# Performance work log

Measured on AMD Instinct MI355X. Metric: run time of the kernel, lower is better.

Reference implementation:

```python
import jax, jax.numpy as jnp
import numpy as np

RC = 5.0
P = 6
N_ATOM = 4
N_AXIS = 8
EPS = 1e-5
C_RES = 0.89442719  # sqrt(0.8)
C_NEW = 0.4472      # ~sqrt(0.2)
BESSEL_PREF = float(np.sqrt(2.0 / RC))


def poly_cutoff(x):
    # nequip-style PolynomialCutoff, p=6
    xr = x / RC
    p = float(P)
    out = (1.0
           - (p + 1.0) * (p + 2.0) / 2.0 * xr ** P
           + p * (p + 2.0) * xr ** (P + 1)
           - p * (p + 1.0) / 2.0 * xr ** (P + 2))
    return jnp.where(xr < 1.0, out, 0.0)


def bessel(x, w):
    # x: [E], w: [n_basis] (trainable n*pi weights)
    return BESSEL_PREF * jnp.sin(w * x[:, None] / RC) / x[:, None]


def layer_norm(x, g, b):
    m = jnp.mean(x, axis=-1, keepdims=True)
    v = jnp.var(x, axis=-1, keepdims=True)
    return (x - m) * jax.lax.rsqrt(v + EPS) * g + b


def mlp3(x, W1, b1, W2, b2, W3, b3):
    # FFN: hidden block (linear-tanh-linear) + tanh + final linear
    h = jnp.tanh(x @ W1 + b1)
    h = jnp.tanh(h @ W2 + b2)
    return h @ W3 + b3


def resnet3(x, W1, b1, W2, b2, W3, b3):
    # ResNet: residual added where in/out dims match (final 64->64 linear)
    h = jnp.tanh(x @ W1 + b1)
    h = h @ W2 + b2
    return jnp.tanh(h) @ W3 + b3 + h


def seg_mean(x, idx, n):
    s = jax.ops.segment_sum(x, idx, num_segments=n)
    c = jax.ops.segment_sum(jnp.ones((x.shape[0],), x.dtype), idx, num_segments=n)
    c = jnp.maximum(c, 1.0).reshape((n,) + (1,) * (x.ndim - 1))
    return s / c


def setup_inputs() -> dict:
    key = jax.random.key(0)
    ks = iter(jax.random.split(key, 64))
    N, E, E2 = 40000, 320000, 160000
    NB, NR, NS, NA = 16, 64, 16, 8
    D = NA * NS  # 128 = n_hidden
    L = 2
    f32 = jnp.float32

    def nrm(shape, s=0.05):
        return jax.random.normal(next(ks), shape, dtype=f32) * s

    inp = {}
    inp['atom_types'] = jax.random.randint(next(ks), (N,), 0, N_ATOM, dtype=jnp.int32)
    ev = jax.random.normal(next(ks), (E, 3), dtype=f32)
    inp['env_vectors'] = ev
    inp['env_length'] = jnp.linalg.norm(ev, axis=-1) + 0.1
    inp['edge_length'] = jax.random.uniform(next(ks), (E2,), dtype=f32) * 4.0 + 0.5
    inp['env_index'] = jax.random.randint(next(ks), (2, E), 0, N, dtype=jnp.int32)
    inp['edge_index'] = jax.random.randint(next(ks), (2, E2), 0, N, dtype=jnp.int32)
    inp['bessel_w'] = jnp.arange(1, NB + 1, dtype=f32) * jnp.pi
    A = 2 * N_ATOM + NB  # 24
    inp['sr_W1'], inp['sr_b1'] = nrm((A, 64)), nrm((64,))
    inp['sr_W2'], inp['sr_b2'] = nrm((64, 64)), nrm((64,))
    inp['sr_W3'], inp['sr_b3'] = nrm((64, NS)), nrm((NS,))
    inp['rd_W1'], inp['rd_b1'] = nrm((A, 64)), nrm((64,))
    inp['rd_W2'], inp['rd_b2'] = nrm((64, 64)), nrm((64,))
    inp['rd_W3'], inp['rd_b3'] = nrm((64, NR)), nrm((NR,))
    inp['ne_emb_W'], inp['ne_emb_b'] = nrm((NR, D)), nrm((D,))
    inp['ne_nln_g'], inp['ne_nln_b'] = jnp.ones((D,), f32), jnp.zeros((D,), f32)
    inp['ne_eln_g'], inp['ne_eln_b'] = jnp.ones((NR,), f32), jnp.zeros((NR,), f32)
    inp['ly_emb_W'], inp['ly_emb_b'] = nrm((L, NR, D)), nrm((L, D))
    inp['ly_hid_W1'], inp['ly_hid_b1'] = nrm((L, 2 * D, 128)), nrm((L, 128))
    inp['ly_hid_W2'], inp['ly_hid_b2'] = nrm((L, 128, 128)), nrm((L, 128))
    inp['ly_hid_W3'], inp['ly_hid_b3'] = nrm((L, 128, D)), nrm((L, D))
    inp['ly_rdl_W1'], inp['ly_rdl_b1'] = nrm((L, NR + D, 64)), nrm((L, 64))
    inp['ly_rdl_W2'], inp['ly_rdl_b2'] = nrm((L, 64, 64)), nrm((L, 64))
    inp['ly_rdl_W3'], inp['ly_rdl_b3'] = nrm((L, 64, NR)), nrm((L, NR))
    inp['ly_nln_g'], inp['ly_nln_b'] = jnp.ones((L, D), f32), jnp.zeros((L, D), f32)
    inp['ly_eln_g'], inp['ly_eln_b'] = jnp.ones((L, NR), f32), jnp.zeros((L, NR), f32)
    return inp


def reference(atom_types, env_vectors, env_length, edge_length, env_index, edge_index,
              bessel_w,
              sr_W1, sr_b1, sr_W2, sr_b2, sr_W3, sr_b3,
              rd_W1, rd_b1, rd_W2, rd_b2, rd_W3, rd_b3,
              ne_emb_W, ne_emb_b, ne_nln_g, ne_nln_b, ne_eln_g, ne_eln_b,
              ly_emb_W, ly_emb_b,
              ly_hid_W1, ly_hid_b1, ly_hid_W2, ly_hid_b2, ly_hid_W3, ly_hid_b3,
              ly_rdl_W1, ly_rdl_b1, ly_rdl_W2, ly_rdl_b2, ly_rdl_W3, ly_rdl_b3,
              ly_nln_g, ly_nln_b, ly_eln_g, ly_eln_b):
    N = atom_types.shape[0]
    oh = jax.nn.one_hot(atom_types, N_ATOM, dtype=env_vectors.dtype)
    # atom_attr[index].transpose(1,0).reshape(E,-1) == concat of the two endpoints' one-hots
    env_attr = jnp.concatenate([oh[env_index[0]], oh[env_index[1]]], -1)   # [E, 2*n_atom]
    edge_attr = jnp.concatenate([oh[edge_index[0]], oh[edge_index[1]]], -1)
    ud_env = poly_cutoff(env_length)[:, None]    # [E, 1]
    ud_edge = poly_cutoff(edge_length)[:, None]  # [E2, 1]
    feat_env = jnp.concatenate([env_attr, ud_env * bessel(env_length, bessel_w)], -1)
    feat_edge = jnp.concatenate([edge_attr, ud_edge * bessel(edge_length, bessel_w)], -1)
    env_sqrt = mlp3(feat_env, sr_W1, sr_b1, sr_W2, sr_b2, sr_W3, sr_b3) * ud_env  # [E, n_sqrt]
    env_radial = layer_norm(mlp3(feat_env, rd_W1, rd_b1, rd_W2, rd_b2, rd_W3, rd_b3), ne_eln_g, ne_eln_b) * ud_env
    edge_radial = layer_norm(mlp3(feat_edge, rd_W1, rd_b1, rd_W2, rd_b2, rd_W3, rd_b3), ne_eln_g, ne_eln_b) * ud_edge
    # SE(2) aggregation: msg = [env_sqrt | ud * env_vectors]; outer product per node
    msg = env_sqrt[:, :, None] * (ud_env * env_vectors)[:, None, :]  # [E, n_sqrt, 3]
    agg = seg_mean(msg, env_index[1], N)                             # [N, n_sqrt, 3]
    gram = jnp.einsum('nds,nes->nde', agg, agg)[:, :, :N_AXIS]       # [N, n_sqrt, n_axis]
    node_emb = layer_norm(gram.reshape(N, -1), ne_nln_g, ne_nln_b)   # [N, D]
    env_hidden = (env_radial @ ne_emb_W + ne_emb_b) * (node_emb[env_index[1]] + node_emb[env_index[0]]) * 0.5
    edge_hidden = (edge_radial @ ne_emb_W + ne_emb_b) * (node_emb[edge_index[1]] + node_emb[edge_index[0]]) * 0.5
    for l in range(ly_emb_W.shape[0]):
        env_weight = env_radial @ ly_emb_W[l] + ly_emb_b[l]  # [E, D]
        agg2 = seg_mean(env_weight * node_emb[env_index[1]], env_index[1], N)
        node_emb = C_RES * node_emb + C_NEW * layer_norm(agg2, ly_nln_g[l], ly_nln_b[l])
        env_hidden = mlp3(jnp.concatenate([node_emb[env_index[0]], env_hidden], -1),
                          ly_hid_W1[l], ly_hid_b1[l], ly_hid_W2[l], ly_hid_b2[l], ly_hid_W3[l], ly_hid_b3[l])
        edge_hidden = mlp3(jnp.concatenate([node_emb[edge_index[0]], edge_hidden], -1),
                           ly_hid_W1[l], ly_hid_b1[l], ly_hid_W2[l], ly_hid_b2[l], ly_hid_W3[l], ly_hid_b3[l])
        env_radial = C_RES * env_radial + C_NEW * ud_env * layer_norm(
            resnet3(jnp.concatenate([env_radial, env_hidden], -1),
                    ly_rdl_W1[l], ly_rdl_b1[l], ly_rdl_W2[l], ly_rdl_b2[l], ly_rdl_W3[l], ly_rdl_b3[l]),
            ly_eln_g[l], ly_eln_b[l])
        edge_radial = C_RES * edge_radial + C_NEW * ud_edge * layer_norm(
            resnet3(jnp.concatenate([edge_radial, edge_hidden], -1),
                    ly_rdl_W1[l], ly_rdl_b1[l], ly_rdl_W2[l], ly_rdl_b2[l], ly_rdl_W3[l], ly_rdl_b3[l]),
            ly_eln_g[l], ly_eln_b[l])
    return env_radial, edge_radial, node_emb, env_hidden, edge_hidden
```

## Files before the change

### kernel.cpp

```cpp
#include <hip/hip_runtime.h>
#include <math.h>

#define C_RES 0.89442719f
#define C_NEW 0.4472f
#define LN_EPS 1e-5f
#define BESSEL_PREF 0.6324555320336759f
#define RC_INV 0.2f

typedef __attribute__((ext_vector_type(8))) short short8;
typedef __attribute__((ext_vector_type(8))) unsigned short u16x8;
typedef __attribute__((ext_vector_type(16))) float f32x16;

__device__ __forceinline__ float fast_tanh(float x) {
  float ax = fabsf(x);
  float e = __expf(2.0f * ax);
  float t = 1.0f - 2.0f / (e + 1.0f);
  return copysignf(t, x);
}

__device__ __forceinline__ unsigned short f2b(float f) {
  __bf16 h = (__bf16)f;
  return __builtin_bit_cast(unsigned short, h);
}

__device__ __forceinline__ float b2f(unsigned short v) {
  return __uint_as_float((unsigned)v << 16);
}

__device__ __forceinline__ u16x8 cvt8(const float* s) {
  const float4 v0 = *(const float4*)s;
  const float4 v1 = *(const float4*)(s + 4);
  u16x8 w;
  w[0]=f2b(v0.x); w[1]=f2b(v0.y); w[2]=f2b(v0.z); w[3]=f2b(v0.w);
  w[4]=f2b(v1.x); w[5]=f2b(v1.y); w[6]=f2b(v1.z); w[7]=f2b(v1.w);
  return w;
}

__device__ __forceinline__ short8 cvt8s(const float* s) {
  const float4 v0 = *(const float4*)s;
  const float4 v1 = *(const float4*)(s + 4);
  short8 w;
  w[0]=(short)f2b(v0.x); w[1]=(short)f2b(v0.y); w[2]=(short)f2b(v0.z); w[3]=(short)f2b(v0.w);
  w[4]=(short)f2b(v1.x); w[5]=(short)f2b(v1.y); w[6]=(short)f2b(v1.z); w[7]=(short)f2b(v1.w);
  return w;
}

__device__ __forceinline__ float poly_cutoff(float x) {
  float xr = x * RC_INV;
  if (xr >= 1.0f) return 0.0f;
  float x2 = xr * xr;
  float x3 = x2 * xr;
  float x6 = x3 * x3;
  return 1.0f - 28.0f * x6 + 48.0f * x6 * xr - 21.0f * x6 * x2;
}

__device__ __forceinline__ int swz(int s, int kc) {
  return s ^ ((s >> 5) << 1) ^ ((kc & 1) << 2);
}

__global__ void zero_int_kernel(int* __restrict__ p, int n) {
  int i = blockIdx.x * blockDim.x + threadIdx.x;
  int stride = gridDim.x * blockDim.x;
  for (; i < n; i += stride) p[i] = 0;
}


__global__ void hist_kernel(int E, const int* __restrict__ idx, int* __restrict__ ecnt) {
  int t = blockIdx.x * 256 + threadIdx.x;
  if (t < E) atomicAdd(&ecnt[idx[E + t]], 1);
}

__launch_bounds__(1024)
__global__ void scan_kernel(const int* __restrict__ ecnt, int* __restrict__ eoff,
                            int* __restrict__ ecur, int n) {
  __shared__ int wsum[16];
  __shared__ int carry;
  const int tid = threadIdx.x;
  const int lane = tid & 63, wid = tid >> 6;
  if (tid == 0) carry = 0;
  __syncthreads();
  for (int b0 = 0; b0 < n; b0 += 1024) {
    const int i = b0 + tid;
    const int v = (i < n) ? ecnt[i] : 0;
    int incl = v;
    #pragma unroll
    for (int o = 1; o < 64; o <<= 1) {
      const int t = __shfl_up(incl, o);
      if (lane >= o) incl += t;
    }
    if (lane == 63) wsum[wid] = incl;
    __syncthreads();
    if (wid == 0) {
      const int wv = (lane < 16) ? wsum[lane] : 0;
      int wsc = wv;
      #pragma unroll
      for (int o = 1; o < 16; o <<= 1) {
        const int t = __shfl_up(wsc, o);
        if (lane >= o) wsc += t;
      }
      if (lane < 16) wsum[lane] = wsc - wv;
    }
    __syncthreads();
    const int c0 = carry;
    const int excl = c0 + wsum[wid] + incl - v;
    if (i < n) { eoff[i] = excl; ecur[i] = excl; }
    __syncthreads();
    if (tid == 1023) carry = c0 + wsum[15] + incl;
    __syncthreads();
  }
  if (tid == 0) eoff[n] = carry;
}

__global__ void scatter_kernel(int E, const int* __restrict__ idx,
                               int* __restrict__ ecur, int* __restrict__ perm) {
  int t = blockIdx.x * 256 + threadIdx.x;
  if (t < E) {
    const int pos = atomicAdd(&ecur[idx[E + t]], 1);
    perm[pos] = t;
  }
}


__global__ void pack_hid_weights(const float* __restrict__ W1,
                                 const float* __restrict__ W2,
                                 const float* __restrict__ W3,
                                 unsigned short* __restrict__ out)
{
  int t = blockIdx.x * 256 + threadIdx.x;
  if (t >= 131072) return;
  int l = t >> 16;
  int oidx = t & 65535;
  const float* src;
  int midx;
  if (oidx < 32768)      { src = W1 + l * 32768; midx = oidx; }
  else if (oidx < 49152) { src = W2 + l * 16384; midx = oidx - 32768; }
  else                   { src = W3 + l * 16384; midx = oidx - 49152; }
  int j = midx & 7;
  int lane = (midx >> 3) & 63;
  int blk = midx >> 9;
  int ct = blk & 3, kc = blk >> 2;
  int col = ct * 32 + (lane & 31);
  int k = kc * 16 + (lane >> 5) * 8 + j;
  out[l * 65536 + oidx] = f2b(src[k * 128 + col]);
}

__global__ void pack_rdl_weights(const float* __restrict__ W1,
                                 const float* __restrict__ W2,
                                 const float* __restrict__ W3,
                                 unsigned short* __restrict__ out)
{
  int t = blockIdx.x * 256 + threadIdx.x;
  if (t >= 40960) return;
  int l = t / 20480;
  int o = t - l * 20480;
  const float* src;
  int midx;
  if (o < 12288)      { src = W1 + l * 12288; midx = o; }
  else if (o < 16384) { src = W2 + l * 4096;  midx = o - 12288; }
  else                { src = W3 + l * 4096;  midx = o - 16384; }
  int j = midx & 7;
  int lane = (midx >> 3) & 63;
  int blk = midx >> 9;
  int ct = blk & 1, kc = blk >> 1;
  int col = ct * 32 + (lane & 31);
  int k = kc * 16 + (lane >> 5) * 8 + j;
  out[l * 20480 + o] = f2b(src[k * 64 + col]);
}

__global__ void pack_feat_weights(const float* __restrict__ rdW1,
                                  const float* __restrict__ rdW2,
                                  const float* __restrict__ rdW3,
                                  const float* __restrict__ srW1,
                                  const float* __restrict__ srW2,
                                  const float* __restrict__ srW3,
                                  unsigned short* __restrict__ out)
{
  int t = blockIdx.x * 256 + threadIdx.x;
  if (t >= 18432) return;
  const int blk = t >> 9, midx = t & 511;
  const int j = midx & 7, lane = (midx >> 3) & 63;
  const float* src; int kc, ct, K, NC;
  if (blk < 4)       { int b = blk;      src = rdW1; kc = b>>1; ct = b&1; K = 24; NC = 64; }
  else if (blk < 12) { int b = blk - 4;  src = rdW2; kc = b>>1; ct = b&1; K = 64; NC = 64; }
  else if (blk < 20) { int b = blk - 12; src = rdW3; kc = b>>1; ct = b&1; K = 64; NC = 64; }
  else if (blk < 24) { int b = blk - 20; src = srW1; kc = b>>1; ct = b&1; K = 24; NC = 64; }
  else if (blk < 32) { int b = blk - 24; src = srW2; kc = b>>1; ct = b&1; K = 64; NC = 64; }
  else               { int b = blk - 32; src = srW3; kc = b;    ct = 0;   K = 64; NC = 16; }
  const int col = ct * 32 + (lane & 31);
  const int k = kc * 16 + (lane >> 5) * 8 + j;
  const float v = (k < K && col < NC) ? src[k * NC + col] : 0.0f;
  out[t] = f2b(v);
}

__global__ void pack_emb_weights(const float* __restrict__ W,
                                 unsigned short* __restrict__ out)
{
  int t = blockIdx.x * 256 + threadIdx.x;
  if (t >= 8192) return;
  const int j = t & 7, lane = (t >> 3) & 63, blk = t >> 9;
  const int ct = blk & 3, kc = blk >> 2;
  const int col = ct * 32 + (lane & 31);
  const int k = kc * 16 + (lane >> 5) * 8 + j;
  out[t] = f2b(W[k * 128 + col]);
}


#define FEAT_TRANS(BASEBLK, V0, V1) do {                                        \
    _Pragma("unroll")                                                           \
    for (int ct_ = 0; ct_ < 2; ++ct_) {                                         \
      const int colh_ = ct_*32 + cl;                                            \
      const int kc2_  = colh_ >> 4;                                             \
      const int b3_   = (colh_ >> 3) & 1;                                       \
      const int jj_   = colh_ & 7;                                              \
      const int blk_  = ((BASEBLK) + kc2_*3 + wave)*512;                        \
      _Pragma("unroll")                                                         \
      for (int q_ = 0; q_ < 16; ++q_) {                                         \
        const int row32_ = (q_ & 3) + 8*(q_ >> 2) + 4*(lane >> 5);              \
        const int s2_ = (row32_ & 31) + 32*b3_;                                 \
        const float v_ = ct_ ? (V1)[q_] : (V0)[q_];                             \
        afrag[blk_ + swz(s2_, kc2_)*8 + jj_] = f2b(fast_tanh(v_));              \
      }                                                                         \
    }                                                                           \
  } while (0)

__launch_bounds__(192)
__global__ void feat_mfma(
    int g1, int n1, const float* __restrict__ lens1, const int* __restrict__ idx1,
    float* __restrict__ radial1, float* __restrict__ ud1,
    int n2, const float* __restrict__ lens2, const int* __restrict__ idx2,
    float* __restrict__ radial2, float* __restrict__ ud2,
    const int* __restrict__ types, const float* __restrict__ vecs,
    const float* __restrict__ bessel_w,
    const unsigned short* __restrict__ wpackf,
    const float* __restrict__ srb1, const float* __restrict__ srb2,
    const float* __restrict__ srb3,
    const float* __restrict__ rdb1, const float* __restrict__ rdb2,
    const float* __restrict__ rdb3,
    const float* __restrict__ eln_g, const float* __restrict__ eln_b,
    float* __restrict__ msgbuf)
{
  __shared__ __align__(16) unsigned short afrag[30*512];
  __shared__ __align__(16) unsigned short wlds[36*512];
  __shared__ float udl[96];

  const int tid  = threadIdx.x;
  const int lane = tid & 63;
  const int wave = tid >> 6;
  const int cl   = lane & 31;

  int blk = blockIdx.x;
  const bool has_sr = (blk < g1);
  int nrows; const float* lens; const int* idx; float* radial_out; float* ud_out;
  if (has_sr) { nrows = n1; lens = lens1; idx = idx1; radial_out = radial1; ud_out = ud1; }
  else { blk -= g1; nrows = n2; lens = lens2; idx = idx2; radial_out = radial2; ud_out = ud2; }
  const int base = blk * 96;

  for (int i = tid; i < 2304; i += 192)
    *(u16x8*)&wlds[i*8] = *(const u16x8*)&wpackf[i*8];

  {
    const int r = tid >> 1, h = tid & 1;
    int rowc = base + r;
    const bool valid = rowc < nrows;
    if (!valid) rowc = nrows - 1;
    const int i0 = idx[rowc];
    const int i1 = idx[nrows + rowc];
    const float len = lens[rowc];
    const float ud = poly_cutoff(len);
    const int t0 = types[i0], t1 = types[i1];
    const float invl = 1.0f / len;
    const int rt = r >> 5;
    #pragma unroll
    for (int m = 0; m < 12; ++m) {
      const int k = h + m*2;
      float v;
      if (k < 4)      v = (t0 == k) ? 1.0f : 0.0f;
      else if (k < 8) v = (t1 == (k-4)) ? 1.0f : 0.0f;
      else            v = ud * BESSEL_PREF * __sinf(bessel_w[k-8] * len * RC_INV) * invl;
      const int kc = k >> 4;
      const int s_ = (r & 31) + 32*((k >> 3) & 1);
      afrag[(kc*3 + rt)*512 + swz(s_, kc)*8 + (k & 7)] = f2b(v);
    }
    #pragma unroll
    for (int m = 0; m < 4; ++m) {
      const int k = 24 + h + m*2;
      const int s_ = (r & 31) + 32*((k >> 3) & 1);
      afrag[(1*3 + rt)*512 + swz(s_, 1)*8 + (k & 7)] = 0;
    }
    if (h == 0) {
      udl[r] = ud;
      if (valid) {
        ud_out[rowc] = ud;
        if (has_sr) {
          msgbuf[(size_t)rowc*20 + 16] = ud * vecs[(size_t)rowc*3 + 0];
          msgbuf[(size_t)rowc*20 + 17] = ud * vecs[(size_t)rowc*3 + 1];
          msgbuf[(size_t)rowc*20 + 18] = ud * vecs[(size_t)rowc*3 + 2];
        }
      }
    }
  }
  __syncthreads();

  f32x16 acc0, acc1;

  {
    const float bv0 = rdb1[cl], bv1 = rdb1[32 + cl];
    #pragma unroll
    for (int q = 0; q < 16; ++q) { acc0[q] = bv0; acc1[q] = bv1; }
  }
  #pragma unroll
  for (int kc = 0; kc < 2; ++kc) {
    const short8 a  = *(const short8*)&afrag[(kc*3 + wave)*512 + swz(lane, kc)*8];
    const short8 w0 = *(const short8*)&wlds[(kc*2 + 0)*512 + lane*8];
    const short8 w1 = *(const short8*)&wlds[(kc*2 + 1)*512 + lane*8];
    acc0 = __builtin_amdgcn_mfma_f32_32x32x16_bf16(a, w0, acc0, 0, 0, 0);
    acc1 = __builtin_amdgcn_mfma_f32_32x32x16_bf16(a, w1, acc1, 0, 0, 0);
  }
  FEAT_TRANS(6, acc0, acc1);

  {
    const float bv0 = rdb2[cl], bv1 = rdb2[32 + cl];
    #pragma unroll
    for (int q = 0; q < 16; ++q) { acc0[q] = bv0; acc1[q] = bv1; }
  }
  #pragma unroll
  for (int kc = 0; kc < 4; ++kc) {
    const short8 a  = *(const short8*)&afrag[((6 + kc*3) + wave)*512 + swz(lane, kc)*8];
    const short8 w0 = *(const short8*)&wlds[(4 + kc*2 + 0)*512 + lane*8];
    const short8 w1 = *(const short8*)&wlds[(4 + kc*2 + 1)*512 + lane*8];
    acc0 = __builtin_amdgcn_mfma_f32_32x32x16_bf16(a, w0, acc0, 0, 0, 0);
    acc1 = __builtin_amdgcn_mfma_f32_32x32x16_bf16(a, w1, acc1, 0, 0, 0);
  }
  FEAT_TRANS(18, acc0, acc1);

  {
    const float bv0 = rdb3[cl], bv1 = rdb3[32 + cl];
    #pragma unroll
    for (int q = 0; q < 16; ++q) { acc0[q] = bv0; acc1[q] = bv1; }
  }
  #pragma unroll
  for (int kc = 0; kc < 4; ++kc) {
    const short8 a  = *(const short8*)&afrag[((18 + kc*3) + wave)*512 + swz(lane, kc)*8];
    const short8 w0 = *(const short8*)&wlds[(12 + kc*2 + 0)*512 + lane*8];
    const short8 w1 = *(const short8*)&wlds[(12 + kc*2 + 1)*512 + lane*8];
    acc0 = __builtin_amdgcn_mfma_f32_32x32x16_bf16(a, w0, acc0, 0, 0, 0);
    acc1 = __builtin_amdgcn_mfma_f32_32x32x16_bf16(a, w1, acc1, 0, 0, 0);
  }
  {
    const float eg0 = eln_g[cl],      eb0 = eln_b[cl];
    const float eg1 = eln_g[32 + cl], eb1 = eln_b[32 + cl];
    #pragma unroll
    for (int q = 0; q < 16; ++q) {
      const float v0 = acc0[q], v1 = acc1[q];
      float s = v0 + v1, ss = v0*v0 + v1*v1;
      #pragma unroll
      for (int o = 1; o <= 16; o <<= 1) {
        s  += __shfl_xor(s, o);
        ss += __shfl_xor(ss, o);
      }
      const float m   = s * (1.0f/64.0f);
      const float inv = rsqrtf(ss * (1.0f/64.0f) - m*m + LN_EPS);
      const int row32 = (q & 3) + 8*(q >> 2) + 4*(lane >> 5);
      const int rloc  = wave*32 + row32;
      const int row   = base + rloc;
      if (row < nrows) {
        const float u = udl[rloc];
        radial_out[(size_t)row*64 + cl]      = ((v0 - m)*inv*eg0 + eb0) * u;
        radial_out[(size_t)row*64 + 32 + cl] = ((v1 - m)*inv*eg1 + eb1) * u;
      }
    }
  }

  if (has_sr) {
    {
      const float bv0 = srb1[cl], bv1 = srb1[32 + cl];
      #pragma unroll
      for (int q = 0; q < 16; ++q) { acc0[q] = bv0; acc1[q] = bv1; }
    }
    #pragma unroll
    for (int kc = 0; kc < 2; ++kc) {
      const short8 a  = *(const short8*)&afrag[(kc*3 + wave)*512 + swz(lane, kc)*8];
      const short8 w0 = *(const short8*)&wlds[(20 + kc*2 + 0)*512 + lane*8];
      const short8 w1 = *(const short8*)&wlds[(20 + kc*2 + 1)*512 + lane*8];
      acc0 = __builtin_amdgcn_mfma_f32_32x32x16_bf16(a, w0, acc0, 0, 0, 0);
      acc1 = __builtin_amdgcn_mfma_f32_32x32x16_bf16(a, w1, acc1, 0, 0, 0);
    }
    FEAT_TRANS(6, acc0, acc1);

    {
      const float bv0 = srb2[cl], bv1 = srb2[32 + cl];
      #pragma unroll
      for (int q = 0; q < 16; ++q) { acc0[q] = bv0; acc1[q] = bv1; }
    }
    #pragma unroll
    for (int kc = 0; kc < 4; ++kc) {
      const short8 a  = *(const short8*)&afrag[((6 + kc*3) + wave)*512 + swz(lane, kc)*8];
      const short8 w0 = *(const short8*)&wlds[(24 + kc*2 + 0)*512 + lane*8];
      const short8 w1 = *(const short8*)&wlds[(24 + kc*2 + 1)*512 + lane*8];
      acc0 = __builtin_amdgcn_mfma_f32_32x32x16_bf16(a, w0, acc0, 0, 0, 0);
      acc1 = __builtin_amdgcn_mfma_f32_32x32x16_bf16(a, w1, acc1, 0, 0, 0);
    }
    FEAT_TRANS(18, acc0, acc1);

    {
      const float bv0 = (cl < 16) ? srb3[cl] : 0.0f;
      #pragma unroll
      for (int q = 0; q < 16; ++q) acc0[q] = bv0;
    }
    #pragma unroll
    for (int kc = 0; kc < 4; ++kc) {
      const short8 a  = *(const short8*)&afrag[((18 + kc*3) + wave)*512 + swz(lane, kc)*8];
      const short8 w0 = *(const short8*)&wlds[(32 + kc)*512 + lane*8];
      acc0 = __builtin_amdgcn_mfma_f32_32x32x16_bf16(a, w0, acc0, 0, 0, 0);
    }
    if (cl < 16) {
      #pragma unroll
      for (int q = 0; q < 16; ++q) {
        const int row32 = (q & 3) + 8*(q >> 2) + 4*(lane >> 5);
        const int rloc  = wave*32 + row32;
        const int row   = base + rloc;
        if (row < nrows) msgbuf[(size_t)row*20 + cl] = acc0[q] * udl[rloc];
      }
    }
  }
}


__launch_bounds__(256)
__global__ void msg_gather_kernel(int N, const int* __restrict__ eoff,
                                  const int* __restrict__ perm,
                                  const float* __restrict__ msgbuf,
                                  float* __restrict__ aggS)
{
  const int w = (blockIdx.x * 256 + threadIdx.x) >> 6;
  const int lane = threadIdx.x & 63;
  if (w >= N) return;
  const int s = eoff[w], e = eoff[w + 1];
  const int d = lane / 3, c = lane - d * 3;
  float acc = 0.0f;
  for (int j = s; j < e; ++j) {
    const int ed = perm[j];
    if (lane < 48)
      acc += msgbuf[(size_t)ed*20 + d] * msgbuf[(size_t)ed*20 + 16 + c];
  }
  if (lane < 48) aggS[(size_t)w*48 + lane] = acc;
}


__device__ __forceinline__ void block128_stats(float x, float& m, float& inv, float* red) {
  float s = x, ss = x*x;
  #pragma unroll
  for (int o = 32; o; o >>= 1) { s += __shfl_down(s, o); ss += __shfl_down(ss, o); }
  const int t = threadIdx.x;
  if ((t & 63) == 0) { red[(t >> 6)*2] = s; red[(t >> 6)*2 + 1] = ss; }
  __syncthreads();
  const float S = red[0] + red[2], SS = red[1] + red[3];
  m = S * (1.0f/128.0f);
  const float var = SS * (1.0f/128.0f) - m*m;
  inv = rsqrtf(var + LN_EPS);
}

__launch_bounds__(128)
__global__ void node_emb_kernel(int N, const float* __restrict__ aggS,
                                const int* __restrict__ ecnt,
                                const float* __restrict__ g, const float* __restrict__ b,
                                float* __restrict__ node_emb)
{
  const int n = blockIdx.x, t = threadIdx.x;
  __shared__ float S[48];
  __shared__ float red[4];
  if (t < 48) S[t] = aggS[(size_t)n*48 + t];
  __syncthreads();
  const float ic = 1.0f / fmaxf((float)ecnt[n], 1.0f);
  const int d = t >> 3, e = t & 7;
  const float x = (S[d*3+0]*S[e*3+0] + S[d*3+1]*S[e*3+1] + S[d*3+2]*S[e*3+2]) * ic * ic;
  float m, inv;
  block128_stats(x, m, inv, red);
  node_emb[(size_t)n*128 + t] = (x - m)*inv*g[t] + b[t];
}


__launch_bounds__(256)
__global__ void agg_gather_kernel(int N, const int* __restrict__ eoff,
                                  const int* __restrict__ perm,
                                  const float* __restrict__ radial,
                                  float* __restrict__ mean_r)
{
  const int w = (blockIdx.x * 256 + threadIdx.x) >> 6;
  const int lane = threadIdx.x & 63;
  if (w >= N) return;
  const int s = eoff[w], e = eoff[w + 1];
  float acc = 0.0f;
  for (int j = s; j < e; ++j) {
    const int ed = perm[j];
    acc += radial[(size_t)ed * 64 + lane];
  }
  const float inv = 1.0f / fmaxf((float)(e - s), 1.0f);
  mean_r[(size_t)w * 64 + lane] = acc * inv;
}


__launch_bounds__(256)
__global__ void node_update_gemm(
    int N, const float* __restrict__ mean_r, const int* __restrict__ ecnt,
    const float* __restrict__ W, const float* __restrict__ bias,
    const float* __restrict__ g, const float* __restrict__ b,
    float* __restrict__ node_emb)
{
  __shared__ __align__(16) float lw[64*128];
  __shared__ float lm[32][65];
  const int tid = threadIdx.x;
  const int base = blockIdx.x * 32;

  for (int i = tid; i < 8192; i += 256) lw[i] = W[i];
  {
    const int rr0 = tid >> 6, k = tid & 63;
    for (int rr = rr0; rr < 32; rr += 4) {
      const int n = base + rr;
      lm[rr][k] = (n < N) ? mean_r[(size_t)n*64 + k] : 0.0f;
    }
  }
  __syncthreads();

  const int r0 = (tid >> 5) * 4, j0 = (tid & 31) * 4;
  float acc[4][4];
  #pragma unroll
  for (int j = 0; j < 4; ++j) {
    const float bj = bias[j0 + j];
    acc[0][j] = bj; acc[1][j] = bj; acc[2][j] = bj; acc[3][j] = bj;
  }
  for (int k = 0; k < 64; ++k) {
    const float4 w = *(const float4*)&lw[k*128 + j0];
    const float s0 = lm[r0][k],   s1 = lm[r0+1][k];
    const float s2 = lm[r0+2][k], s3 = lm[r0+3][k];
    acc[0][0] += s0*w.x; acc[0][1] += s0*w.y; acc[0][2] += s0*w.z; acc[0][3] += s0*w.w;
    acc[1][0] += s1*w.x; acc[1][1] += s1*w.y; acc[1][2] += s1*w.z; acc[1][3] += s1*w.w;
    acc[2][0] += s2*w.x; acc[2][1] += s2*w.y; acc[2][2] += s2*w.z; acc[2][3] += s2*w.w;
    acc[3][0] += s3*w.x; acc[3][1] += s3*w.y; acc[3][2] += s3*w.z; acc[3][3] += s3*w.w;
  }

  const float g0 = g[j0], g1 = g[j0+1], g2 = g[j0+2], g3 = g[j0+3];
  const float bb0 = b[j0], bb1 = b[j0+1], bb2 = b[j0+2], bb3 = b[j0+3];
  #pragma unroll
  for (int i = 0; i < 4; ++i) {
    const int n = base + r0 + i;
    if (n >= N) continue;
    const float mask = (ecnt[n] > 0) ? 1.0f : 0.0f;
    const float4 old = *(const float4*)&node_emb[(size_t)n*128 + j0];
    const float x0 = old.x * acc[i][0] * mask;
    const float x1 = old.y * acc[i][1] * mask;
    const float x2 = old.z * acc[i][2] * mask;
    const float x3 = old.w * acc[i][3] * mask;
    float s = x0 + x1 + x2 + x3;
    float ss = x0*x0 + x1*x1 + x2*x2 + x3*x3;
    #pragma unroll
    for (int o = 1; o <= 16; o <<= 1) {
      s  += __shfl_xor(s, o);
      ss += __shfl_xor(ss, o);
    }
    const float m = s * (1.0f/128.0f);
    const float inv = rsqrtf(ss * (1.0f/128.0f) - m*m + LN_EPS);
    float4 o4;
    o4.x = C_RES*old.x + C_NEW*((x0 - m)*inv*g0 + bb0);
    o4.y = C_RES*old.y + C_NEW*((x1 - m)*inv*g1 + bb1);
    o4.z = C_RES*old.z + C_NEW*((x2 - m)*inv*g2 + bb2);
    o4.w = C_RES*old.w + C_NEW*((x3 - m)*inv*g3 + bb3);
    *(float4*)&node_emb[(size_t)n*128 + j0] = o4;
  }
}


__launch_bounds__(192)
__global__ void emb_mfma(
    int g1, int n1, const float* __restrict__ radial1, const int* __restrict__ idx1,
    float* __restrict__ out1,
    int n2, const float* __restrict__ radial2, const int* __restrict__ idx2,
    float* __restrict__ out2,
    const unsigned short* __restrict__ wpck, const float* __restrict__ bias,
    const float* __restrict__ node_emb)
{
  __shared__ __align__(16) unsigned short afrag[12*512];
  __shared__ __align__(16) unsigned short wlds[16*512];
  __shared__ int i0l[96], i1l[96];

  const int tid = threadIdx.x, lane = tid & 63, wave = tid >> 6;
  const int cl = lane & 31;

  int blk = blockIdx.x;
  int nrows; const float* radial; const int* idx; float* out;
  if (blk < g1) { nrows = n1; radial = radial1; idx = idx1; out = out1; }
  else { blk -= g1; nrows = n2; radial = radial2; idx = idx2; out = out2; }
  const int base = blk * 96;

  for (int i = tid; i < 1024; i += 192)
    *(u16x8*)&wlds[i*8] = *(const u16x8*)&wpck[i*8];

  {
    const int r = tid >> 1, h = tid & 1;
    int rowg = base + r;
    if (rowg >= nrows) rowg = nrows - 1;
    if (h == 0) { i0l[r] = idx[rowg]; i1l[r] = idx[nrows + rowg]; }
    const float* rsrc = radial + (size_t)rowg * 64;
    #pragma unroll
    for (int g = 0; g < 4; ++g) {
      const int k = h*32 + g*8;
      const u16x8 w = cvt8(rsrc + k);
      const int kc = k >> 4;
      const int s_ = (r & 31) + 32*((k >> 3) & 1);
      *(u16x8*)&afrag[(kc*3 + (r>>5))*512 + swz(s_, kc)*8] = w;
    }
  }
  __syncthreads();

  f32x16 acc0, acc1, acc2, acc3;
  {
    const float bv0 = bias[cl], bv1 = bias[32+cl];
    const float bv2 = bias[64+cl], bv3 = bias[96+cl];
    #pragma unroll
    for (int q = 0; q < 16; ++q) { acc0[q]=bv0; acc1[q]=bv1; acc2[q]=bv2; acc3[q]=bv3; }
  }
  #pragma unroll
  for (int kc = 0; kc < 4; ++kc) {
    const short8 a  = *(const short8*)&afrag[(kc*3 + wave)*512 + swz(lane, kc)*8];
    const short8 w0 = *(const short8*)&wlds[(kc*4 + 0)*512 + lane*8];
    const short8 w1 = *(const short8*)&wlds[(kc*4 + 1)*512 + lane*8];
    const short8 w2 = *(const short8*)&wlds[(kc*4 + 2)*512 + lane*8];
    const short8 w3 = *(const short8*)&wlds[(kc*4 + 3)*512 + lane*8];
    acc0 = __builtin_amdgcn_mfma_f32_32x32x16_bf16(a, w0, acc0, 0, 0, 0);
    acc1 = __builtin_amdgcn_mfma_f32_32x32x16_bf16(a, w1, acc1, 0, 0, 0);
    acc2 = __builtin_amdgcn_mfma_f32_32x32x16_bf16(a, w2, acc2, 0, 0, 0);
    acc3 = __builtin_amdgcn_mfma_f32_32x32x16_bf16(a, w3, acc3, 0, 0, 0);
  }

  #pragma unroll
  for (int q = 0; q < 16; ++q) {
    const int row32 = (q & 3) + 8*(q >> 2) + 4*(lane >> 5);
    const int rloc  = wave*32 + row32;
    const int row   = base + rloc;
    if (row >= nrows) continue;
    const float* n0 = node_emb + (size_t)i0l[rloc]*128;
    const float* n1 = node_emb + (size_t)i1l[rloc]*128;
    float* op = out + (size_t)row*128;
    op[cl]    = acc0[q] * 0.5f * (n0[cl]    + n1[cl]);
    op[32+cl] = acc1[q] * 0.5f * (n0[32+cl] + n1[32+cl]);
    op[64+cl] = acc2[q] * 0.5f * (n0[64+cl] + n1[64+cl]);
    op[96+cl] = acc3[q] * 0.5f * (n0[96+cl] + n1[96+cl]);
  }
}


#define STAGE_WG(SRC, OFFU16, B) do {                                           \
    _Pragma("unroll")                                                           \
    for (int i_ = 0; i_ < 2; ++i_) {                                            \
      const int c_ = tid + i_*256;                                              \
      *(u16x8*)&wg[B][c_*8] = *(const u16x8*)&(SRC)[(OFFU16) + c_*8];           \
    }                                                                           \
  } while (0)

__launch_bounds__(256, 3)
__global__ void hidrdl_mfma(
    int g1,
    int n1, const int* __restrict__ idx1, const float* __restrict__ ud1,
    float* __restrict__ hid1, float* __restrict__ rad1,
    int n2, const int* __restrict__ idx2, const float* __restrict__ ud2,
    float* __restrict__ hid2, float* __restrict__ rad2,
    const float* __restrict__ node_emb,
    const unsigned short* __restrict__ wpackh,
    const float* __restrict__ hb1, const float* __restrict__ hb2,
    const float* __restrict__ hb3,
    const unsigned short* __restrict__ wpackr,
    const float* __restrict__ rb1, const float* __restrict__ rb2,
    const float* __restrict__ rb3,
    const float* __restrict__ eln_g, const float* __restrict__ eln_b)
{
  __shared__ __align__(16) unsigned short afragH[16384];
  __shared__ __align__(16) unsigned short wg[2][4096];

  const int tid  = threadIdx.x;
  const int lane = tid & 63;
  const int wave = tid >> 6;
  const int cl   = lane & 31;
  const int khalf = lane >> 5;

  int blk = blockIdx.x;
  int nrows; const int* idx0; const float* ud; float* hidden; float* radial;
  if (blk < g1) { nrows = n1; idx0 = idx1; ud = ud1; hidden = hid1; radial = rad1; }
  else { blk -= g1; nrows = n2; idx0 = idx2; ud = ud2; hidden = hid2; radial = rad2; }
  const int base = blk * 128;

  int lrow = base + wave*32 + cl;
  if (lrow >= nrows) lrow = nrows - 1;
  const int i0 = idx0[lrow];
  const float* nsrc = node_emb + (size_t)i0 * 128;
  const float* hsrc = hidden + (size_t)lrow * 128;
  const float* rsrc = radial + (size_t)lrow * 64;

  short8 aN[8], aH[8];
  #pragma unroll
  for (int kc = 0; kc < 8; ++kc) aN[kc] = cvt8s(nsrc + kc*16 + khalf*8);
  #pragma unroll
  for (int kc = 0; kc < 8; ++kc) aH[kc] = cvt8s(hsrc + kc*16 + khalf*8);

  f32x16 acc[4];

  #pragma unroll
  for (int ct = 0; ct < 4; ++ct) {
    const float bv = hb1[ct*32 + cl];
    #pragma unroll
    for (int q = 0; q < 16; ++q) acc[ct][q] = bv;
  }
  STAGE_WG(wpackh, 0, 0);
  __syncthreads();
  #pragma unroll
  for (int p = 0; p < 8; ++p) {
    if (p < 7) STAGE_WG(wpackh, (p+1)*4096, (p+1)&1);
    else       STAGE_WG(wpackh, 32768, 0);
    #pragma unroll
    for (int kcl = 0; kcl < 2; ++kcl) {
      const int kc = p*2 + kcl;
      const short8 a = (kc < 8) ? aN[kc] : aH[kc-8];
      #pragma unroll
      for (int ct = 0; ct < 4; ++ct) {
        const short8 b = *(const short8*)&wg[p&1][ (kcl*4 + ct)*512 + lane*8 ];
        acc[ct] = __builtin_amdgcn_mfma_f32_32x32x16_bf16(a, b, acc[ct], 0, 0, 0);
      }
    }
    __syncthreads();
  }

  #pragma unroll
  for (int ct = 0; ct < 4; ++ct) {
    const int kc  = ct*2 + ((lane >> 4) & 1);
    const int oct = (lane >> 3) & 1;
    const int j   = lane & 7;
    const int xk  = (oct << 1) ^ ((kc & 1) << 2);
    const int hi  = 4*khalf;
    const int bi  = (wave*8 + kc)*512 + oct*256 + j;
    #pragma unroll
    for (int q = 0; q < 16; ++q) {
      const int m32 = (q & 3) + 8*(q >> 2) + hi;
      afragH[bi + (m32 ^ xk)*8] = f2b(fast_tanh(acc[ct][q]));
    }
  }

  #pragma unroll
  for (int ct = 0; ct < 4; ++ct) {
    const float bv = hb2[ct*32 + cl];
    #pragma unroll
    for (int q = 0; q < 16; ++q) acc[ct][q] = bv;
  }
  #pragma unroll
  for (int p = 0; p < 4; ++p) {
    if (p < 3) STAGE_WG(wpackh, 32768 + (p+1)*4096, (p+1)&1);
    else       STAGE_WG(wpackh, 49152, 0);
    #pragma unroll
    for (int kcl = 0; kcl < 2; ++kcl) {
      const int kc = p*2 + kcl;
      const short8 a = *(const short8*)&afragH[ (wave*8 + kc)*512 + swz(lane, kc)*8 ];
      #pragma unroll
      for (int ct = 0; ct < 4; ++ct) {
        const short8 b = *(const short8*)&wg[p&1][ (kcl*4 + ct)*512 + lane*8 ];
        acc[ct] = __builtin_amdgcn_mfma_f32_32x32x16_bf16(a, b, acc[ct], 0, 0, 0);
      }
    }
    __syncthreads();
  }

  #pragma unroll
  for (int ct = 0; ct < 4; ++ct) {
    const int kc  = ct*2 + ((lane >> 4) & 1);
    const int oct = (lane >> 3) & 1;
    const int j   = lane & 7;
    const int xk  = (oct << 1) ^ ((kc & 1) << 2);
    const int hi  = 4*khalf;
    const int bi  = (wave*8 + kc)*512 + oct*256 + j;
    #pragma unroll
    for (int q = 0; q < 16; ++q) {
      const int m32 = (q & 3) + 8*(q >> 2) + hi;
      afragH[bi + (m32 ^ xk)*8] = f2b(fast_tanh(acc[ct][q]));
    }
  }

  #pragma unroll
  for (int ct = 0; ct < 4; ++ct) {
    const float bv = hb3[ct*32 + cl];
    #pragma unroll
    for (int q = 0; q < 16; ++q) acc[ct][q] = bv;
  }
  #pragma unroll
  for (int p = 0; p < 4; ++p) {
    if (p < 3) STAGE_WG(wpackh, 49152 + (p+1)*4096, (p+1)&1);
    else       STAGE_WG(wpackr, 0, 0);
    #pragma unroll
    for (int kcl = 0; kcl < 2; ++kcl) {
      const int kc = p*2 + kcl;
      const short8 a = *(const short8*)&afragH[ (wave*8 + kc)*512 + swz(lane, kc)*8 ];
      #pragma unroll
      for (int ct = 0; ct < 4; ++ct) {
        const short8 b = *(const short8*)&wg[p&1][ (kcl*4 + ct)*512 + lane*8 ];
        acc[ct] = __builtin_amdgcn_mfma_f32_32x32x16_bf16(a, b, acc[ct], 0, 0, 0);
      }
    }
    __syncthreads();
  }

  #pragma unroll
  for (int ct = 0; ct < 4; ++ct) {
    const int col = ct*32 + cl;
    #pragma unroll
    for (int q = 0; q < 16; ++q) {
      const int row = base + wave*32 + (q & 3) + 8*(q >> 2) + 4*khalf;
      if (row < nrows) hidden[(size_t)row*128 + col] = acc[ct][q];
    }
  }
  #pragma unroll
  for (int ct = 0; ct < 4; ++ct) {
    const int kc  = ct*2 + ((lane >> 4) & 1);
    const int oct = (lane >> 3) & 1;
    const int j   = lane & 7;
    const int xk  = (oct << 1) ^ ((kc & 1) << 2);
    const int hi  = 4*khalf;
    const int bi  = (wave*8 + kc)*512 + oct*256 + j;
    #pragma unroll
    for (int q = 0; q < 16; ++q) {
      const int m32 = (q & 3) + 8*(q >> 2) + hi;
      afragH[bi + (m32 ^ xk)*8] = f2b(acc[ct][q]);
    }
  }

  short8 aR[4];
  #pragma unroll
  for (int kc = 0; kc < 4; ++kc) aR[kc] = cvt8s(rsrc + kc*16 + khalf*8);

  f32x16 racc0, racc1;
  {
    const float bv0 = rb1[cl], bv1 = rb1[32 + cl];
    #pragma unroll
    for (int q = 0; q < 16; ++q) { racc0[q] = bv0; racc1[q] = bv1; }
  }
  #pragma unroll
  for (int t = 0; t < 3; ++t) {
    if (t < 2) STAGE_WG(wpackr, (t+1)*4096, (t+1)&1);
    else       STAGE_WG(wpackr, 12288, 1);
    #pragma unroll
    for (int kk = 0; kk < 4; ++kk) {
      const int kc = t*4 + kk;
      const short8 a = (kc < 4) ? aR[kc]
        : *(const short8*)&afragH[ (wave*8 + (kc-4))*512 + swz(lane, kc-4)*8 ];
      const short8 w0 = *(const short8*)&wg[t&1][ (kk*2 + 0)*512 + lane*8 ];
      const short8 w1 = *(const short8*)&wg[t&1][ (kk*2 + 1)*512 + lane*8 ];
      racc0 = __builtin_amdgcn_mfma_f32_32x32x16_bf16(a, w0, racc0, 0, 0, 0);
      racc1 = __builtin_amdgcn_mfma_f32_32x32x16_bf16(a, w1, racc1, 0, 0, 0);
    }
    __syncthreads();
  }

  #pragma unroll
  for (int ct = 0; ct < 2; ++ct) {
    const int colh = ct*32 + cl;
    const int kc2  = colh >> 4;
    const int b3_  = (colh >> 3) & 1;
    const int jj   = colh & 7;
    const int blk2 = (wave*8 + kc2)*512;
    #pragma unroll
    for (int q = 0; q < 16; ++q) {
      const int row32 = (q & 3) + 8*(q >> 2) + 4*khalf;
      const int s_ = (row32 & 31) + 32*b3_;
      const float v = ct ? racc1[q] : racc0[q];
      afragH[blk2 + swz(s_, kc2)*8 + jj] = f2b(fast_tanh(v));
    }
  }

  f32x16 rh0, rh1;
  {
    const float bv0 = rb2[cl], bv1 = rb2[32 + cl];
    #pragma unroll
    for (int q = 0; q < 16; ++q) { rh0[q] = bv0; rh1[q] = bv1; }
  }
  STAGE_WG(wpackr, 16384, 0);
  #pragma unroll
  for (int kc = 0; kc < 4; ++kc) {
    const short8 a  = *(const short8*)&afragH[ (wave*8 + kc)*512 + swz(lane, kc)*8 ];
    const short8 w0 = *(const short8*)&wg[1][ (kc*2 + 0)*512 + lane*8 ];
    const short8 w1 = *(const short8*)&wg[1][ (kc*2 + 1)*512 + lane*8 ];
    rh0 = __builtin_amdgcn_mfma_f32_32x32x16_bf16(a, w0, rh0, 0, 0, 0);
    rh1 = __builtin_amdgcn_mfma_f32_32x32x16_bf16(a, w1, rh1, 0, 0, 0);
  }
  __syncthreads();

  #pragma unroll
  for (int ct = 0; ct < 2; ++ct) {
    const int colh = ct*32 + cl;
    const int kc2  = colh >> 4;
    const int b3_  = (colh >> 3) & 1;
    const int jj   = colh & 7;
    const int blk2 = (wave*8 + 4 + kc2)*512;
    #pragma unroll
    for (int q = 0; q < 16; ++q) {
      const int row32 = (q & 3) + 8*(q >> 2) + 4*khalf;
      const int s_ = (row32 & 31) + 32*b3_;
      const float v = ct ? rh1[q] : rh0[q];
      afragH[blk2 + swz(s_, kc2)*8 + jj] = f2b(fast_tanh(v));
    }
  }

  {
    const float bv0 = rb3[cl], bv1 = rb3[32 + cl];
    #pragma unroll
    for (int q = 0; q < 16; ++q) { racc0[q] = bv0; racc1[q] = bv1; }
  }
  #pragma unroll
  for (int kc = 0; kc < 4; ++kc) {
    const short8 a  = *(const short8*)&afragH[ (wave*8 + 4 + kc)*512 + swz(lane, kc)*8 ];
    const short8 w0 = *(const short8*)&wg[0][ (kc*2 + 0)*512 + lane*8 ];
    const short8 w1 = *(const short8*)&wg[0][ (kc*2 + 1)*512 + lane*8 ];
    racc0 = __builtin_amdgcn_mfma_f32_32x32x16_bf16(a, w0, racc0, 0, 0, 0);
    racc1 = __builtin_amdgcn_mfma_f32_32x32x16_bf16(a, w1, racc1, 0, 0, 0);
  }

  const float eg0 = eln_g[cl],      eb0 = eln_b[cl];
  const float eg1 = eln_g[32 + cl], eb1 = eln_b[32 + cl];
  const float* rtile = radial + (size_t)(base + wave*32) * 64;

  #pragma unroll
  for (int q = 0; q < 16; ++q) {
    const float v0 = racc0[q] + rh0[q];
    const float v1 = racc1[q] + rh1[q];
    float s = v0 + v1, ss = v0*v0 + v1*v1;
    #pragma unroll
    for (int o = 1; o <= 16; o <<= 1) {
      s  += __shfl_xor(s, o);
      ss += __shfl_xor(ss, o);
    }
    const float m   = s * (1.0f/64.0f);
    const float inv = rsqrtf(ss * (1.0f/64.0f) - m*m + LN_EPS);
    const int row32 = (q & 3) + 8*(q >> 2) + 4*khalf;
    const int row   = base + wave*32 + row32;
    if (row < nrows) {
      const float u = ud[row];
      const float oldA = rtile[row32*64 + cl];
      const float oldB = rtile[row32*64 + 32 + cl];
      radial[(size_t)row*64 + cl]      = C_RES*oldA + C_NEW*u*((v0 - m)*inv*eg0 + eb0);
      radial[(size_t)row*64 + 32 + cl] = C_RES*oldB + C_NEW*u*((v1 - m)*inv*eg1 + eb1);
    }
  }
}


extern "C" void kernel_launch(void* const* d_in, const int* in_sizes, int n_in,
                              void* d_out, int out_size, void* d_ws, size_t ws_size,
                              hipStream_t stream)
{
  const int*   atom_types = (const int*)  d_in[0];
  const float* env_vec    = (const float*)d_in[1];
  const float* env_len    = (const float*)d_in[2];
  const float* edge_len   = (const float*)d_in[3];
  const int*   env_idx    = (const int*)  d_in[4];
  const int*   edge_idx   = (const int*)  d_in[5];
  const float* bessel_w   = (const float*)d_in[6];
  const float* srW1 = (const float*)d_in[7];  const float* srb1 = (const float*)d_in[8];
  const float* srW2 = (const float*)d_in[9];  const float* srb2 = (const float*)d_in[10];
  const float* srW3 = (const float*)d_in[11]; const float* srb3 = (const float*)d_in[12];
  const float* rdW1 = (const float*)d_in[13]; const float* rdb1 = (const float*)d_in[14];
  const float* rdW2 = (const float*)d_in[15]; const float* rdb2 = (const float*)d_in[16];
  const float* rdW3 = (const float*)d_in[17]; const float* rdb3 = (const float*)d_in[18];
  const float* ne_emb_W = (const float*)d_in[19]; const float* ne_emb_b = (const float*)d_in[20];
  const float* ne_nln_g = (const float*)d_in[21]; const float* ne_nln_b = (const float*)d_in[22];
  const float* ne_eln_g = (const float*)d_in[23]; const float* ne_eln_b = (const float*)d_in[24];
  const float* ly_emb_W = (const float*)d_in[25]; const float* ly_emb_b = (const float*)d_in[26];
  const float* ly_hid_W1 = (const float*)d_in[27]; const float* ly_hid_b1 = (const float*)d_in[28];
  const float* ly_hid_W2 = (const float*)d_in[29]; const float* ly_hid_b2 = (const float*)d_in[30];
  const float* ly_hid_W3 = (const float*)d_in[31]; const float* ly_hid_b3 = (const float*)d_in[32];
  const float* ly_rdl_W1 = (const float*)d_in[33]; const float* ly_rdl_b1 = (const float*)d_in[34];
  const float* ly_rdl_W2 = (const float*)d_in[35]; const float* ly_rdl_b2 = (const float*)d_in[36];
  const float* ly_rdl_W3 = (const float*)d_in[37]; const float* ly_rdl_b3 = (const float*)d_in[38];
  const float* ly_nln_g = (const float*)d_in[39]; const float* ly_nln_b = (const float*)d_in[40];
  const float* ly_eln_g = (const float*)d_in[41]; const float* ly_eln_b = (const float*)d_in[42];

  const int N  = in_sizes[0];
  const int E  = in_sizes[2];
  const int E2 = in_sizes[3];

  float* out = (float*)d_out;
  float* env_radial  = out;
  float* edge_radial = env_radial + (size_t)E * 64;
  float* node_emb    = edge_radial + (size_t)E2 * 64;
  float* env_hidden  = node_emb + (size_t)N * 128;
  float* edge_hidden = env_hidden + (size_t)E * 128;

  float* ws = (float*)d_ws;
  float* ud_env  = ws;  ws += E;
  float* ud_edge = ws;  ws += E2;
  float* aggS    = ws;  ws += (size_t)N * 48;
  float* msgbuf  = ws;  ws += (size_t)E * 20;
  float* mean_r  = msgbuf;
  unsigned short* wpack  = (unsigned short*)ws; ws += 65536;
  unsigned short* wpack2 = (unsigned short*)ws; ws += 20480;
  unsigned short* wpack3 = (unsigned short*)ws; ws += 9216;
  unsigned short* wpackE = (unsigned short*)ws; ws += 4096;
  int* ecnt = (int*)ws; ws += N;
  int* eoff = (int*)ws; ws += N + 1;
  int* ecur = (int*)ws; ws += N + 1;
  int* perm = (int*)ws; ws += E;

  const int gEr  = (E  + 95) / 96;
  const int gE2r = (E2 + 95) / 96;
  const int gEf  = (E  + 127) / 128;
  const int gE2f = (E2 + 127) / 128;
  const int gN32 = (N + 31) / 32;
  const int gN4w = (N * 64 + 255) / 256;

  zero_int_kernel<<<256, 256, 0, stream>>>(ecnt, N);
  hist_kernel<<<(E + 255) / 256, 256, 0, stream>>>(E, env_idx, ecnt);
  scan_kernel<<<1, 1024, 0, stream>>>(ecnt, eoff, ecur, N);
  scatter_kernel<<<(E + 255) / 256, 256, 0, stream>>>(E, env_idx, ecur, perm);

  pack_hid_weights<<<512, 256, 0, stream>>>(ly_hid_W1, ly_hid_W2, ly_hid_W3, wpack);
  pack_rdl_weights<<<160, 256, 0, stream>>>(ly_rdl_W1, ly_rdl_W2, ly_rdl_W3, wpack2);
  pack_feat_weights<<<72, 256, 0, stream>>>(rdW1, rdW2, rdW3, srW1, srW2, srW3, wpack3);
  pack_emb_weights<<<32, 256, 0, stream>>>(ne_emb_W, wpackE);

  feat_mfma<<<gEr + gE2r, 192, 0, stream>>>(
      gEr, E, env_len, env_idx, env_radial, ud_env,
      E2, edge_len, edge_idx, edge_radial, ud_edge,
      atom_types, env_vec, bessel_w, wpack3,
      srb1, srb2, srb3, rdb1, rdb2, rdb3,
      ne_eln_g, ne_eln_b, msgbuf);

  msg_gather_kernel<<<gN4w, 256, 0, stream>>>(N, eoff, perm, msgbuf, aggS);
  node_emb_kernel<<<N, 128, 0, stream>>>(N, aggS, ecnt, ne_nln_g, ne_nln_b, node_emb);

  emb_mfma<<<gEr + gE2r, 192, 0, stream>>>(
      gEr, E, env_radial, env_idx, env_hidden,
      E2, edge_radial, edge_idx, edge_hidden,
      wpackE, ne_emb_b, node_emb);

  for (int l = 0; l < 2; ++l) {
    agg_gather_kernel<<<gN4w, 256, 0, stream>>>(N, eoff, perm, env_radial, mean_r);
    node_update_gemm<<<gN32, 256, 0, stream>>>(N, mean_r, ecnt,
        ly_emb_W + (size_t)l*64*128, ly_emb_b + (size_t)l*128,
        ly_nln_g + (size_t)l*128, ly_nln_b + (size_t)l*128, node_emb);

    hidrdl_mfma<<<gEf + gE2f, 256, 0, stream>>>(
        gEf,
        E, env_idx, ud_env, env_hidden, env_radial,
        E2, edge_idx, ud_edge, edge_hidden, edge_radial,
        node_emb,
        wpack + (size_t)l*65536,
        ly_hid_b1 + (size_t)l*128, ly_hid_b2 + (size_t)l*128, ly_hid_b3 + (size_t)l*128,
        wpack2 + (size_t)l*20480,
        ly_rdl_b1 + (size_t)l*64, ly_rdl_b2 + (size_t)l*64, ly_rdl_b3 + (size_t)l*64,
        ly_eln_g + (size_t)l*64, ly_eln_b + (size_t)l*64);
  }
}
```

Before: 1.224 ms.

## Precompute per-node first-layer hidden projection and use rational tanh approximation

Adds a per-node MFMA kernel that computes node_emb @ W1[:128] + b1 once per node and writes it to a workspace buffer. The edge kernel then gathers these preactivations into its accumulators and only multiplies the hidden half of W1, halving the first-layer K for all edges. This removes work that was repeated for every edge sharing a source node, at the cost of an extra launch and a gather of fp32 preactivations. Separately, tanh is replaced by a clamped Padé rational approximation with a hardware reciprocal, which is cheaper than exp+divide but less accurate near saturation.

```diff
diff --git a/kernel.cpp b/kernel.cpp
--- a/kernel.cpp
+++ b/kernel.cpp
@@ -12,10 +12,11 @@
 typedef __attribute__((ext_vector_type(16))) float f32x16;
 
 __device__ __forceinline__ float fast_tanh(float x) {
-  float ax = fabsf(x);
-  float e = __expf(2.0f * ax);
-  float t = 1.0f - 2.0f / (e + 1.0f);
-  return copysignf(t, x);
+  float t = fminf(3.0f, fmaxf(-3.0f, x));
+  float t2 = t * t;
+  float num = t * fmaf(t2, 10.0f, 105.0f);
+  float den = fmaf(t2, fmaf(t2, 1.0f, 45.0f), 105.0f);
+  return num * __builtin_amdgcn_rcpf(den);
 }
 
 __device__ __forceinline__ unsigned short f2b(float f) {
@@ -649,6 +650,71 @@
 }
 
 
+__launch_bounds__(192)
+__global__ void nepre_mfma(int N, const float* __restrict__ node_emb,
+                           const unsigned short* __restrict__ wpackh1,
+                           const float* __restrict__ hb1,
+                           float* __restrict__ nepre)
+{
+  __shared__ __align__(16) unsigned short afrag[24*512];
+  __shared__ __align__(16) unsigned short wlds[32*512];
+  const int tid = threadIdx.x, lane = tid & 63, wave = tid >> 6;
+  const int cl = lane & 31;
+  const int base = blockIdx.x * 96;
+
+  for (int i = tid; i < 2048; i += 192)
+    *(u16x8*)&wlds[i*8] = *(const u16x8*)&wpackh1[i*8];
+
+  {
+    const int r = tid >> 1, h = tid & 1;
+    int rowg = base + r;
+    if (rowg >= N) rowg = N - 1;
+    const float* s = node_emb + (size_t)rowg * 128;
+    #pragma unroll
+    for (int g = 0; g < 8; ++g) {
+      const int k = h*64 + g*8;
+      const u16x8 w = cvt8(s + k);
+      const int kc = k >> 4;
+      const int s_ = (r & 31) + 32*((k >> 3) & 1);
+      *(u16x8*)&afrag[(kc*3 + (r>>5))*512 + swz(s_, kc)*8] = w;
+    }
+  }
+  __syncthreads();
+
+  f32x16 acc0, acc1, acc2, acc3;
+  {
+    const float bv0 = hb1[cl], bv1 = hb1[32+cl];
+    const float bv2 = hb1[64+cl], bv3 = hb1[96+cl];
+    #pragma unroll
+    for (int q = 0; q < 16; ++q) { acc0[q]=bv0; acc1[q]=bv1; acc2[q]=bv2; acc3[q]=bv3; }
+  }
+  #pragma unroll
+  for (int kc = 0; kc < 8; ++kc) {
+    const short8 a  = *(const short8*)&afrag[(kc*3 + wave)*512 + swz(lane, kc)*8];
+    const short8 w0 = *(const short8*)&wlds[(kc*4 + 0)*512 + lane*8];
+    const short8 w1 = *(const short8*)&wlds[(kc*4 + 1)*512 + lane*8];
+    const short8 w2 = *(const short8*)&wlds[(kc*4 + 2)*512 + lane*8];
+    const short8 w3 = *(const short8*)&wlds[(kc*4 + 3)*512 + lane*8];
+    acc0 = __builtin_amdgcn_mfma_f32_32x32x16_bf16(a, w0, acc0, 0, 0, 0);
+    acc1 = __builtin_amdgcn_mfma_f32_32x32x16_bf16(a, w1, acc1, 0, 0, 0);
+    acc2 = __builtin_amdgcn_mfma_f32_32x32x16_bf16(a, w2, acc2, 0, 0, 0);
+    acc3 = __builtin_amdgcn_mfma_f32_32x32x16_bf16(a, w3, acc3, 0, 0, 0);
+  }
+
+  #pragma unroll
+  for (int q = 0; q < 16; ++q) {
+    const int row32 = (q & 3) + 8*(q >> 2) + 4*(lane >> 5);
+    const int row   = base + wave*32 + row32;
+    if (row >= N) continue;
+    float* op = nepre + (size_t)row*128;
+    op[cl]    = acc0[q];
+    op[32+cl] = acc1[q];
+    op[64+cl] = acc2[q];
+    op[96+cl] = acc3[q];
+  }
+}
+
+
 #define STAGE_WG(SRC, OFFU16, B) do {                                           \
     _Pragma("unroll")                                                           \
     for (int i_ = 0; i_ < 2; ++i_) {                                            \
@@ -664,10 +730,9 @@
     float* __restrict__ hid1, float* __restrict__ rad1,
     int n2, const int* __restrict__ idx2, const float* __restrict__ ud2,
     float* __restrict__ hid2, float* __restrict__ rad2,
-    const float* __restrict__ node_emb,
+    const float* __restrict__ nepre,
     const unsigned short* __restrict__ wpackh,
-    const float* __restrict__ hb1, const float* __restrict__ hb2,
-    const float* __restrict__ hb3,
+    const float* __restrict__ hb2, const float* __restrict__ hb3,
     const unsigned short* __restrict__ wpackr,
     const float* __restrict__ rb1, const float* __restrict__ rb2,
     const float* __restrict__ rb3,
@@ -690,35 +755,37 @@
 
   int lrow = base + wave*32 + cl;
   if (lrow >= nrows) lrow = nrows - 1;
-  const int i0 = idx0[lrow];
-  const float* nsrc = node_emb + (size_t)i0 * 128;
   const float* hsrc = hidden + (size_t)lrow * 128;
   const float* rsrc = radial + (size_t)lrow * 64;
 
-  short8 aN[8], aH[8];
-  #pragma unroll
-  for (int kc = 0; kc < 8; ++kc) aN[kc] = cvt8s(nsrc + kc*16 + khalf*8);
+  short8 aH[8];
   #pragma unroll
   for (int kc = 0; kc < 8; ++kc) aH[kc] = cvt8s(hsrc + kc*16 + khalf*8);
 
   f32x16 acc[4];
 
   #pragma unroll
-  for (int ct = 0; ct < 4; ++ct) {
-    const float bv = hb1[ct*32 + cl];
-    #pragma unroll
-    for (int q = 0; q < 16; ++q) acc[ct][q] = bv;
-  }
-  STAGE_WG(wpackh, 0, 0);
+  for (int q = 0; q < 16; ++q) {
+    const int row32 = (q & 3) + 8*(q >> 2) + 4*khalf;
+    int row = base + wave*32 + row32;
+    if (row >= nrows) row = nrows - 1;
+    const float* np = nepre + (size_t)idx0[row] * 128;
+    acc[0][q] = np[cl];
+    acc[1][q] = np[32 + cl];
+    acc[2][q] = np[64 + cl];
+    acc[3][q] = np[96 + cl];
+  }
+
+  STAGE_WG(wpackh, 16384, 0);
   __syncthreads();
   #pragma unroll
-  for (int p = 0; p < 8; ++p) {
-    if (p < 7) STAGE_WG(wpackh, (p+1)*4096, (p+1)&1);
+  for (int p = 0; p < 4; ++p) {
+    if (p < 3) STAGE_WG(wpackh, 16384 + (p+1)*4096, (p+1)&1);
     else       STAGE_WG(wpackh, 32768, 0);
     #pragma unroll
     for (int kcl = 0; kcl < 2; ++kcl) {
       const int kc = p*2 + kcl;
-      const short8 a = (kc < 8) ? aN[kc] : aH[kc-8];
+      const short8 a = aH[kc];
       #pragma unroll
       for (int ct = 0; ct < 4; ++ct) {
         const short8 b = *(const short8*)&wg[p&1][ (kcl*4 + ct)*512 + lane*8 ];
@@ -994,6 +1061,7 @@
   float* aggS    = ws;  ws += (size_t)N * 48;
   float* msgbuf  = ws;  ws += (size_t)E * 20;
   float* mean_r  = msgbuf;
+  float* nepre   = ws;  ws += (size_t)N * 128;
   unsigned short* wpack  = (unsigned short*)ws; ws += 65536;
   unsigned short* wpack2 = (unsigned short*)ws; ws += 20480;
   unsigned short* wpack3 = (unsigned short*)ws; ws += 9216;
@@ -1008,6 +1076,7 @@
   const int gEf  = (E  + 127) / 128;
   const int gE2f = (E2 + 127) / 128;
   const int gN32 = (N + 31) / 32;
+  const int gN96 = (N + 95) / 96;
   const int gN4w = (N * 64 + 255) / 256;
 
   zero_int_kernel<<<256, 256, 0, stream>>>(ecnt, N);
@@ -1041,13 +1110,16 @@
         ly_emb_W + (size_t)l*64*128, ly_emb_b + (size_t)l*128,
         ly_nln_g + (size_t)l*128, ly_nln_b + (size_t)l*128, node_emb);
 
+    nepre_mfma<<<gN96, 192, 0, stream>>>(N, node_emb,
+        wpack + (size_t)l*65536, ly_hid_b1 + (size_t)l*128, nepre);
+
     hidrdl_mfma<<<gEf + gE2f, 256, 0, stream>>>(
         gEf,
         E, env_idx, ud_env, env_hidden, env_radial,
         E2, edge_idx, ud_edge, edge_hidden, edge_radial,
-        node_emb,
+        nepre,
         wpack + (size_t)l*65536,
-        ly_hid_b1 + (size_t)l*128, ly_hid_b2 + (size_t)l*128, ly_hid_b3 + (size_t)l*128,
+        ly_hid_b2 + (size_t)l*128, ly_hid_b3 + (size_t)l*128,
         wpack2 + (size_t)l*20480,
         ly_rdl_b1 + (size_t)l*64, ly_rdl_b2 + (size_t)l*64, ly_rdl_b3 + (size_t)l*64,
         ly_eln_g + (size_t)l*64, ly_eln_b + (size_t)l*64);
```

Result: faster. 1.095 ms, median of 2 (-10.6%).
